# Optimization experiments

Measured on AMD Instinct MI355X. Metric: run time of the kernel, lower is better.

The kernel has to match this reference:

```python
import jax, jax.numpy as jnp
import numpy as np

B, T, DIM = 1, 1024, 1024
H = 8
QLR, KVLR = 768, 512
DNOPE, DROPE, DV = 128, 64, 128
DK = DNOPE + DROPE  # 192
EPS = 1e-5


def _rms(x, w):
    return x * jax.lax.rsqrt(jnp.mean(x * x, axis=-1, keepdims=True) + EPS) * w


def _l2norm(x):
    return x * jax.lax.rsqrt(jnp.sum(x * x, axis=-1, keepdims=True) + 1e-6)


def setup_inputs() -> dict:
    key = jax.random.key(0)
    ks = jax.random.split(key, 12)
    std = 0.02
    rnd = lambda k, shape: (jax.random.normal(k, shape, dtype=jnp.float32) * std)
    return {
        'x': jax.random.normal(ks[0], (B, T, DIM), dtype=jnp.float32),
        'cos': jax.random.normal(ks[1], (T, DROPE), dtype=jnp.float32),
        'sin': jax.random.normal(ks[2], (T, DROPE), dtype=jnp.float32),
        'wq_a': rnd(ks[3], (DIM, QLR)),
        'q_norm_w': jnp.ones((QLR,), dtype=jnp.float32),
        'wq_b': rnd(ks[4], (QLR, H * DK)),
        'wkv_a': rnd(ks[5], (DIM, KVLR + DROPE)),
        'kv_norm_w': jnp.ones((KVLR,), dtype=jnp.float32),
        'wkv_b': rnd(ks[6], (KVLR, H * (DNOPE + DV))),
        'wg_w': rnd(ks[7], (DIM, H * DK)),
        'wg_b': jnp.zeros((H * DK,), dtype=jnp.float32),
        'wb': rnd(ks[8], (DIM, H)),
        'wo': rnd(ks[9], (H * DV, DIM)),
    }


def _kda(q, k, v, g, beta):
    # q,k: [B,T,H,DK]; v: [B,T,H,DV]; g: [B,T,H,DK] (log-decay); beta: [B,T,H]
    q = _l2norm(q) * (DK ** -0.5)
    k = _l2norm(k)
    # time-major for scan
    qs = jnp.moveaxis(q, 1, 0)
    ks_ = jnp.moveaxis(k, 1, 0)
    vs = jnp.moveaxis(v, 1, 0)
    gs = jnp.moveaxis(g, 1, 0)
    bs = jnp.moveaxis(beta, 1, 0)

    def step(S, inp):
        q_t, k_t, v_t, g_t, b_t = inp  # [B,H,DK],[B,H,DK],[B,H,DV],[B,H,DK],[B,H]
        S = S * jnp.exp(g_t)[..., None]                       # per-key-dim decay
        u_t = b_t[..., None] * (v_t - jnp.einsum('bhk,bhkv->bhv', k_t, S))
        S = S + k_t[..., None] * u_t[..., None, :]            # rank-1 delta update
        o_t = jnp.einsum('bhk,bhkv->bhv', q_t, S)
        return S, o_t

    S0 = jnp.zeros((B, H, DK, DV), dtype=q.dtype)
    _, o = jax.lax.scan(step, S0, (qs, ks_, vs, gs, bs))
    return jnp.moveaxis(o, 0, 1)  # [B,T,H,DV]


def reference(x, cos, sin, wq_a, q_norm_w, wq_b, wkv_a, kv_norm_w, wkv_b, wg_w, wg_b, wb, wo):
    # cos/sin are accepted but unused, matching the original forward body.
    q = (_rms(x @ wq_a, q_norm_w) @ wq_b).reshape(B, T, H, DK)
    kv_all = x @ wkv_a
    kv_c, k_pe = kv_all[..., :KVLR], kv_all[..., KVLR:]       # [B,T,KVLR],[B,T,DROPE]
    kv = (_rms(kv_c, kv_norm_w) @ wkv_b).reshape(B, T, H, DNOPE + DV)
    k_nope, v = kv[..., :DNOPE], kv[..., DNOPE:]
    k = jnp.concatenate(
        [k_nope, jnp.broadcast_to(k_pe[:, :, None, :], (B, T, H, DROPE))], axis=-1)
    g = jax.nn.log_sigmoid(x @ wg_w + wg_b).reshape(B, T, H, DK)
    beta = jax.nn.sigmoid(x @ wb).reshape(B, T, H)
    o = _kda(q, k, v, g, beta)
    o = jnp.nan_to_num(o, nan=0.0, posinf=10000.0, neginf=-10000.0)
    return o.reshape(B, T, H * DV) @ wo
```

## Files before the change

### kernel.cpp

```cpp
#include <hip/hip_runtime.h>
#include <hip/hip_bf16.h>
#include <math.h>

#define TT 1024
#define DIM 1024
#define HH 8
#define QLR 768
#define KVLR 512
#define DNOPE 128
#define DROPE 64
#define DV 128
#define DK 192
#define HDK (HH*DK)
#define HKV (HH*(DNOPE+DV))

#define OY   0
#define OQ   3072
#define OC   6144
#define OPL  9984
#define OU   10240
#define OLAM 12288
#define PABLK 12480

typedef __attribute__((ext_vector_type(8))) short short8;
typedef __attribute__((ext_vector_type(4))) float f32x4;

__device__ __forceinline__ unsigned short f2bf_rn(float f) {
    unsigned u = __float_as_uint(f);
    unsigned lsb = (u >> 16) & 1u;
    u += 0x7fffu + lsb;
    return (unsigned short)(u >> 16);
}
__device__ __forceinline__ float bf2f(unsigned short h) {
    return __uint_as_float(((unsigned)h) << 16);
}

__global__ __launch_bounds__(256) void wconv(
    const float* __restrict__ W0, unsigned short* __restrict__ H0,
    unsigned short* __restrict__ L0, int K0, int N0, int T0,
    const float* __restrict__ W1, unsigned short* __restrict__ H1,
    unsigned short* __restrict__ L1, int K1, int N1, int T1,
    const float* __restrict__ W2, unsigned short* __restrict__ H2,
    unsigned short* __restrict__ L2, int K2, int N2, int T2)
{
    __shared__ float Ls[64][65];
    int bx = blockIdx.x;
    const float* W; unsigned short* H; unsigned short* L; int K, N;
    if (bx < T0)           { W = W0; H = H0; L = L0; K = K0; N = N0; }
    else if (bx < T0 + T1) { bx -= T0; W = W1; H = H1; L = L1; K = K1; N = N1; }
    else                   { bx -= T0 + T1; W = W2; H = H2; L = L2; K = K2; N = N2; }

    const int NT = N >> 6;
    const int kt = bx / NT, nt = bx - kt * NT;
    const int k0 = kt * 64, n0 = nt * 64;
    const int tid = threadIdx.x;
    const int r = tid >> 2, c = (tid & 3) * 16;

#pragma unroll
    for (int i = 0; i < 4; i++)
        *(float4*)&Ls[r][c + i * 4] =
            *(const float4*)&W[(size_t)(k0 + r) * N + n0 + c + i * 4];
    __syncthreads();

    const int nr = tid >> 2, kc = (tid & 3) * 16;
    unsigned short hb[16], lb[16];
#pragma unroll
    for (int j = 0; j < 16; j++) {
        float v = Ls[kc + j][nr];
        unsigned short h = f2bf_rn(v);
        hb[j] = h;
        lb[j] = f2bf_rn(v - bf2f(h));
    }
    size_t ob = (size_t)(n0 + nr) * K + k0 + kc;
    *(float4*)&H[ob]     = ((float4*)hb)[0];
    *(float4*)&H[ob + 8] = ((float4*)hb)[1];
    *(float4*)&L[ob]     = ((float4*)lb)[0];
    *(float4*)&L[ob + 8] = ((float4*)lb)[1];
}

__global__ __launch_bounds__(256) void aconv(
    const float* __restrict__ A, unsigned short* __restrict__ H,
    unsigned short* __restrict__ L)
{
    int i = (blockIdx.x * 256 + threadIdx.x) * 8;
    float4 v0 = *(const float4*)&A[i];
    float4 v1 = *(const float4*)&A[i + 4];
    float vv[8] = {v0.x, v0.y, v0.z, v0.w, v1.x, v1.y, v1.z, v1.w};
    unsigned short hb[8], lb[8];
#pragma unroll
    for (int j = 0; j < 8; j++) {
        unsigned short h = f2bf_rn(vv[j]);
        hb[j] = h;
        lb[j] = f2bf_rn(vv[j] - bf2f(h));
    }
    *(float4*)&H[i] = *(float4*)hb;
    *(float4*)&L[i] = *(float4*)lb;
}

__global__ __launch_bounds__(128) void gemm_bt(
    const unsigned short* __restrict__ Ah0, const unsigned short* __restrict__ Al0,
    const unsigned short* __restrict__ Bh0, const unsigned short* __restrict__ Bl0,
    float* __restrict__ C0, int K0, int N0, int T0,
    const unsigned short* __restrict__ Ah1, const unsigned short* __restrict__ Al1,
    const unsigned short* __restrict__ Bh1, const unsigned short* __restrict__ Bl1,
    float* __restrict__ C1, int K1, int N1, int T1,
    const unsigned short* __restrict__ Ah2, const unsigned short* __restrict__ Al2,
    const unsigned short* __restrict__ Bh2, const unsigned short* __restrict__ Bl2,
    float* __restrict__ C2, int K2, int N2, int T2)
{
    __shared__ unsigned short Ahs[64 * 40], Als[64 * 40];
    __shared__ unsigned short Bhs[64 * 40], Bls[64 * 40];

    int bx = blockIdx.x;
    const unsigned short *Ah, *Al, *Bh, *Bl; float* C; int K, N;
    if (bx < T0) {
        Ah = Ah0; Al = Al0; Bh = Bh0; Bl = Bl0; C = C0; K = K0; N = N0;
    } else if (bx < T0 + T1) {
        bx -= T0; Ah = Ah1; Al = Al1; Bh = Bh1; Bl = Bl1; C = C1; K = K1; N = N1;
    } else {
        bx -= T0 + T1; Ah = Ah2; Al = Al2; Bh = Bh2; Bl = Bl2; C = C2; K = K2; N = N2;
    }

    const int tid = threadIdx.x;
    const int w = tid >> 6, l = tid & 63;
    const int q = l >> 4, m16 = l & 15;
    const int bm = blockIdx.y * 64, bn = bx * 64;

    const int c0i = tid * 2, c1i = tid * 2 + 1;
    const int r0 = c0i >> 2, o0 = (c0i & 3) * 8;
    const int r1 = c1i >> 2, o1 = (c1i & 3) * 8;
    const unsigned short* pAh0 = Ah + (size_t)(bm + r0) * K + o0;
    const unsigned short* pAh1 = Ah + (size_t)(bm + r1) * K + o1;
    const unsigned short* pAl0 = Al + (size_t)(bm + r0) * K + o0;
    const unsigned short* pAl1 = Al + (size_t)(bm + r1) * K + o1;
    const unsigned short* pBh0 = Bh + (size_t)(bn + r0) * K + o0;
    const unsigned short* pBh1 = Bh + (size_t)(bn + r1) * K + o1;
    const unsigned short* pBl0 = Bl + (size_t)(bn + r0) * K + o0;
    const unsigned short* pBl1 = Bl + (size_t)(bn + r1) * K + o1;

    f32x4 acc[2][4];
#pragma unroll
    for (int i = 0; i < 2; i++)
#pragma unroll
        for (int j = 0; j < 4; j++)
            acc[i][j] = (f32x4){0.f, 0.f, 0.f, 0.f};

    float4 vAh0 = *(const float4*)pAh0, vAh1 = *(const float4*)pAh1;
    float4 vAl0 = *(const float4*)pAl0, vAl1 = *(const float4*)pAl1;
    float4 vBh0 = *(const float4*)pBh0, vBh1 = *(const float4*)pBh1;
    float4 vBl0 = *(const float4*)pBl0, vBl1 = *(const float4*)pBl1;

    for (int k0 = 0;; k0 += 32) {
        __syncthreads();
        *(float4*)&Ahs[r0 * 40 + o0] = vAh0; *(float4*)&Ahs[r1 * 40 + o1] = vAh1;
        *(float4*)&Als[r0 * 40 + o0] = vAl0; *(float4*)&Als[r1 * 40 + o1] = vAl1;
        *(float4*)&Bhs[r0 * 40 + o0] = vBh0; *(float4*)&Bhs[r1 * 40 + o1] = vBh1;
        *(float4*)&Bls[r0 * 40 + o0] = vBl0; *(float4*)&Bls[r1 * 40 + o1] = vBl1;
        __syncthreads();

        const bool more = (k0 + 32) < K;
        if (more) {
            const int kn = k0 + 32;
            vAh0 = *(const float4*)(pAh0 + kn); vAh1 = *(const float4*)(pAh1 + kn);
            vAl0 = *(const float4*)(pAl0 + kn); vAl1 = *(const float4*)(pAl1 + kn);
            vBh0 = *(const float4*)(pBh0 + kn); vBh1 = *(const float4*)(pBh1 + kn);
            vBl0 = *(const float4*)(pBl0 + kn); vBl1 = *(const float4*)(pBl1 + kn);
        }

        short8 fah[2], fal[2], fbh[4], fbl[4];
#pragma unroll
        for (int mt = 0; mt < 2; mt++) {
            const int row = w * 32 + mt * 16 + m16;
            fah[mt] = *(const short8*)&Ahs[row * 40 + q * 8];
            fal[mt] = *(const short8*)&Als[row * 40 + q * 8];
        }
#pragma unroll
        for (int nt = 0; nt < 4; nt++) {
            const int row = nt * 16 + m16;
            fbh[nt] = *(const short8*)&Bhs[row * 40 + q * 8];
            fbl[nt] = *(const short8*)&Bls[row * 40 + q * 8];
        }
#pragma unroll
        for (int mt = 0; mt < 2; mt++)
#pragma unroll
            for (int nt = 0; nt < 4; nt++) {
                acc[mt][nt] = __builtin_amdgcn_mfma_f32_16x16x32_bf16(
                    fah[mt], fbh[nt], acc[mt][nt], 0, 0, 0);
                acc[mt][nt] = __builtin_amdgcn_mfma_f32_16x16x32_bf16(
                    fah[mt], fbl[nt], acc[mt][nt], 0, 0, 0);
                acc[mt][nt] = __builtin_amdgcn_mfma_f32_16x16x32_bf16(
                    fal[mt], fbh[nt], acc[mt][nt], 0, 0, 0);
            }
        if (!more) break;
    }

#pragma unroll
    for (int mt = 0; mt < 2; mt++)
#pragma unroll
        for (int nt = 0; nt < 4; nt++) {
            const int mrow = bm + w * 32 + mt * 16 + q * 4;
            const int ncol = bn + nt * 16 + m16;
#pragma unroll
            for (int r = 0; r < 4; r++)
                C[(size_t)(mrow + r) * N + ncol] = acc[mt][nt][r];
        }
}

__global__ __launch_bounds__(256) void rmsnorm_bf2(
    const float* __restrict__ in0, const float* __restrict__ w0,
    unsigned short* __restrict__ oh0, unsigned short* __restrict__ ol0,
    const float* __restrict__ in1, const float* __restrict__ w1,
    unsigned short* __restrict__ oh1, unsigned short* __restrict__ ol1)
{
    int bx = blockIdx.x;
    const float* in; const float* w; unsigned short *oh, *ol;
    int t, stride, ncols; float inv_n;
    if (bx < TT) {
        t = bx; in = in0; w = w0; oh = oh0; ol = ol0;
        stride = QLR; ncols = QLR; inv_n = 1.f / QLR;
    } else {
        t = bx - TT; in = in1; w = w1; oh = oh1; ol = ol1;
        stride = KVLR + DROPE; ncols = KVLR; inv_n = 1.f / KVLR;
    }
    const int tid = threadIdx.x;
    const float* row = in + (size_t)t * stride;
    float ss = 0.f;
    for (int c = tid; c < ncols; c += 256) { float v = row[c]; ss += v * v; }
#pragma unroll
    for (int m = 1; m < 64; m <<= 1) ss += __shfl_xor(ss, m);
    __shared__ float red[4];
    if ((tid & 63) == 0) red[tid >> 6] = ss;
    __syncthreads();
    float tot = red[0] + red[1] + red[2] + red[3];
    float scale = rsqrtf(tot * inv_n + 1e-5f);
    for (int c = tid; c < ncols; c += 256) {
        float v = row[c] * scale * w[c];
        unsigned short h = f2bf_rn(v);
        oh[(size_t)t * ncols + c] = h;
        ol[(size_t)t * ncols + c] = f2bf_rn(v - bf2f(h));
    }
}

__global__ __launch_bounds__(256) void small_fused(
    const float* __restrict__ g, const float* __restrict__ bias,
    float* __restrict__ la_h,
    const float* __restrict__ x, const float* __restrict__ wb,
    float* __restrict__ betab,
    const float* __restrict__ qraw, const float* __restrict__ kvb,
    const float* __restrict__ kv_all, float* __restrict__ q_h,
    float* __restrict__ k_h)
{
    int bx = blockIdx.x;
    if (bx < 6144) {
        int i = bx * 256 + threadIdx.x;
        int t = i / HDK, col = i - t * HDK;
        int h = col / DK, d = col - h * DK;
        float z = g[i] + bias[col];
        float la = fminf(z, 0.f) - log1pf(__expf(-fabsf(z)));
        la_h[((size_t)h * TT + t) * DK + d] = la;
        return;
    }
    bx -= 6144;
    const int lane = threadIdx.x & 63, wv = threadIdx.x >> 6;
    if (bx < 2048) {
        const int p = bx * 4 + wv;
        const int t = p >> 3, h = p & 7;
        const float* xr = x + (size_t)t * DIM;
        float s = 0.f;
        for (int e = lane; e < DIM; e += 64) s += xr[e] * wb[e * HH + h];
#pragma unroll
        for (int m = 1; m < 64; m <<= 1) s += __shfl_xor(s, m);
        if (lane == 0) betab[p] = 1.f / (1.f + expf(-s));
        return;
    }
    bx -= 2048;
    {
        const int p = bx * 4 + wv;
        const int t = p >> 3, h = p & 7;

        const float* qrow = qraw + (size_t)t * HDK + h * DK;
        float q0 = qrow[lane], q1 = qrow[lane + 64], q2 = qrow[lane + 128];
        float ss = q0 * q0 + q1 * q1 + q2 * q2;
#pragma unroll
        for (int m = 1; m < 64; m <<= 1) ss += __shfl_xor(ss, m);
        float sc = rsqrtf(ss + 1e-6f) * 0.07216878364870323f;
        float* qo = q_h + ((size_t)h * TT + t) * DK;
        qo[lane] = q0 * sc; qo[lane + 64] = q1 * sc; qo[lane + 128] = q2 * sc;

        const float* knope = kvb + (size_t)t * HKV + h * (DNOPE + DV);
        float k0 = knope[lane], k1 = knope[lane + 64];
        float k2 = kv_all[(size_t)t * (KVLR + DROPE) + KVLR + lane];
        float ks = k0 * k0 + k1 * k1 + k2 * k2;
#pragma unroll
        for (int m = 1; m < 64; m <<= 1) ks += __shfl_xor(ks, m);
        float kc = rsqrtf(ks + 1e-6f);
        float* ko = k_h + ((size_t)h * TT + t) * DK;
        ko[lane] = k0 * kc; ko[lane + 64] = k1 * kc; ko[lane + 128] = k2 * kc;
    }
}

__device__ __forceinline__ float dpp_xor1(float x) {
    return __int_as_float(__builtin_amdgcn_update_dpp(
        0, __float_as_int(x), 0xB1, 0xF, 0xF, false));
}
__device__ __forceinline__ float dpp_xor2(float x) {
    return __int_as_float(__builtin_amdgcn_update_dpp(
        0, __float_as_int(x), 0x4E, 0xF, 0xF, false));
}
__device__ __forceinline__ float dpp_hm(float x) {
    return __int_as_float(__builtin_amdgcn_update_dpp(
        0, __float_as_int(x), 0x141, 0xF, 0xF, false));
}
__device__ __forceinline__ float red16(float x) {
    x += dpp_xor1(x);
    x += dpp_xor2(x);
    x += dpp_hm(x);
    x += __int_as_float(__builtin_amdgcn_update_dpp(0, __float_as_int(x), 0x140, 0xF, 0xF, false));
    return x;
}
__device__ __forceinline__ float red8(float x) {
    x += dpp_xor1(x);
    x += dpp_xor2(x);
    x += dpp_hm(x);
    return x;
}

__device__ __forceinline__ void gl_lds16(const float* g, float* l) {
    __builtin_amdgcn_global_load_lds(
        (const __attribute__((address_space(1))) void*)g,
        (__attribute__((address_space(3))) void*)l, 16, 0, 0);
}
__device__ __forceinline__ void gl_lds4(const float* g, float* l) {
    __builtin_amdgcn_global_load_lds(
        (const __attribute__((address_space(1))) void*)g,
        (__attribute__((address_space(3))) void*)l, 4, 0, 0);
}

__global__ __launch_bounds__(256) void chunk_prep(
    const float* __restrict__ k_h, const float* __restrict__ la_h,
    const float* __restrict__ q_h, const float* __restrict__ kvb,
    const float* __restrict__ betab, float* __restrict__ pa)
{
    __shared__ float Ls[16][196];
    __shared__ float Ks[16][196];
    __shared__ float Qs[16][196];
    __shared__ float Ws[16][196];
    __shared__ float Xs[16][196];
    __shared__ float Ms[16][16];
    __shared__ float bs[16];

    const int tid = threadIdx.x;
    const int n = blockIdx.x >> 3, h = blockIdx.x & 7;
    const size_t g0 = ((size_t)h * TT + n * 16) * DK;
    float* blob = pa + (size_t)blockIdx.x * PABLK;

#pragma unroll
    for (int s = 0; s < 3; s++) {
        int off = (tid * 3 + s) * 4;
        int r = off / 192, c = off - r * 192;
        *(float4*)&Ks[r][c] = *(const float4*)(k_h + g0 + off);
        *(float4*)&Ls[r][c] = *(const float4*)(la_h + g0 + off);
        *(float4*)&Qs[r][c] = *(const float4*)(q_h + g0 + off);
    }
    if (tid < 16) bs[tid] = betab[(size_t)(n * 16 + tid) * HH + h];
    __syncthreads();

    if (tid < 192) {
        float g = 0.f;
#pragma unroll
        for (int i = 0; i < 16; i++) { g += Ls[i][tid]; Ls[i][tid] = g; }
    }
    __syncthreads();

#pragma unroll
    for (int s = 0; s < 12; s++) {
        int idx = s * 256 + tid;
        int i = idx / 192, d = idx - i * 192;
        float G = Ls[i][d];
        float eg = __expf(G), en = __expf(-G);
        float kk = Ks[i][d];
        Ws[i][d] = bs[i] * kk * eg;
        Qs[i][d] *= eg;
        Ks[i][d] = kk * en;
    }
    __syncthreads();

#pragma unroll
    for (int s = 0; s < 3; s++) {
        int off = (tid * 3 + s) * 4;
        int r = off / 192, c = off - r * 192;
        *(float4*)(blob + OQ + off) = *(const float4*)&Qs[r][c];
    }
    if (tid < 192) {
        float lam = __expf(Ls[15][tid]);
        blob[OLAM + tid] = lam;
#pragma unroll
        for (int j4 = 0; j4 < 4; j4++) {
            float4 v;
            v.x = Ks[j4 * 4 + 0][tid] * lam; v.y = Ks[j4 * 4 + 1][tid] * lam;
            v.z = Ks[j4 * 4 + 2][tid] * lam; v.w = Ks[j4 * 4 + 3][tid] * lam;
            *(float4*)(blob + OC + tid * 20 + j4 * 4) = v;
        }
        blob[OC + tid * 20 + 16] = lam;
        blob[OC + tid * 20 + 17] = 0.f;
        blob[OC + tid * 20 + 18] = 0.f; blob[OC + tid * 20 + 19] = 0.f;
    }
    {
        const int i = tid >> 4, j = tid & 15;
        float m = 0.f, p = 0.f;
#pragma unroll
        for (int d4 = 0; d4 < 48; d4++) {
            float4 w  = *(const float4*)&Ws[i][d4 * 4];
            float4 ka = *(const float4*)&Ks[j][d4 * 4];
            float4 qa = *(const float4*)&Qs[i][d4 * 4];
            m += w.x * ka.x + w.y * ka.y + w.z * ka.z + w.w * ka.w;
            p += qa.x * ka.x + qa.y * ka.y + qa.z * ka.z + qa.w * ka.w;
        }
        Ms[i][j] = (j < i) ? m : 0.f;
        blob[OPL + tid] = (j <= i) ? p : 0.f;
    }
    __syncthreads();

    float y[16], uu[16];
    const bool doY = (tid < 192);
    const bool doU = (tid >= 128);
    const int dcol = tid, ccol = tid - 128;
    if (doY) {
#pragma unroll
        for (int i = 0; i < 16; i++) y[i] = Ws[i][dcol];
#pragma unroll
        for (int i = 1; i < 16; i++)
#pragma unroll
            for (int j = 0; j < i; j++)
                y[i] = fmaf(-Ms[i][j], y[j], y[i]);
    }
    if (doU) {
#pragma unroll
        for (int i = 0; i < 16; i++)
            uu[i] = bs[i] * kvb[(size_t)(n * 16 + i) * HKV + h * (DNOPE + DV) + DNOPE + ccol];
#pragma unroll
        for (int i = 1; i < 16; i++)
#pragma unroll
            for (int j = 0; j < i; j++)
                uu[i] = fmaf(-Ms[i][j], uu[j], uu[i]);
    }
    if (doY) {
#pragma unroll
        for (int i = 0; i < 16; i++) Xs[i][dcol] = y[i];
    }
    __syncthreads();
#pragma unroll
    for (int s = 0; s < 3; s++) {
        int off = (tid * 3 + s) * 4;
        int r = off / 192, c = off - r * 192;
        *(float4*)(blob + OY + off) = *(const float4*)&Xs[r][c];
    }
    __syncthreads();
    if (doU) {
#pragma unroll
        for (int i = 0; i < 16; i++) Xs[i][ccol] = uu[i];
    }
    __syncthreads();
#pragma unroll
    for (int s = 0; s < 2; s++) {
        int off = (tid * 2 + s) * 4;
        int r = off / 128, c = off - r * 128;
        *(float4*)(blob + OU + off) = *(const float4*)&Xs[r][c];
    }
}

__global__ __launch_bounds__(256) void kda_chunk(
    const float* __restrict__ pa, unsigned short* __restrict__ obh,
    unsigned short* __restrict__ obl)
{
    __shared__ float Cb[3][3840];
    __shared__ float Pb[3][256];
    __shared__ float ubs[3][32];
    __shared__ float lbs[3][192];
    __shared__ float Ss[392];
    __shared__ float us[40];

    const int tid = threadIdx.x;
    const int w = tid >> 6, lane = tid & 63;
    const int h = blockIdx.x & 7, cg = blockIdx.x >> 3;
    const int c0 = cg * 2;

    const int dg  = tid & 15;
    const int cc  = (tid >> 4) & 1;
    const int tig = tid >> 5;
    const int dbase = dg * 12;

    auto stage = [&](int buf, int n) {
        const float* blob = pa + (size_t)(n * 8 + h) * PABLK;
        if (w == 0) {
#pragma unroll
            for (int s = 0; s < 8; s++)
                gl_lds16(blob + OC + s * 256 + lane * 4, &Cb[buf][s * 256]);
        } else if (w == 1) {
#pragma unroll
            for (int s = 8; s < 15; s++)
                gl_lds16(blob + OC + s * 256 + lane * 4, &Cb[buf][s * 256]);
        } else if (w == 2) {
            gl_lds16(blob + OPL + lane * 4, &Pb[buf][0]);
            if (lane < 32)
                gl_lds4(blob + OU + (lane >> 1) * 128 + c0 + (lane & 1), &ubs[buf][0]);
            if (lane < 48)
                gl_lds16(blob + OLAM + lane * 4, &lbs[buf][0]);
        }
    };

    auto ldYQ = [&](int n, float4 (&Y)[2][3], float4 (&Q)[2][3]) {
        const float* blob = pa + (size_t)(n * 8 + h) * PABLK;
#pragma unroll
        for (int i = 0; i < 2; i++) {
            const float* py = blob + OY + (tig * 2 + i) * 192 + dbase;
            const float* pq = blob + OQ + (tig * 2 + i) * 192 + dbase;
#pragma unroll
            for (int s = 0; s < 3; s++) {
                Y[i][s] = *(const float4*)(py + s * 4);
                Q[i][s] = *(const float4*)(pq + s * 4);
            }
        }
    };

    for (int idx = tid; idx < 392; idx += 256) Ss[idx] = 0.f;
    stage(0, 0);
    stage(1, 1);

    float4 YA[2][3], QA[2][3], YB[2][3], QB[2][3];
    ldYQ(0, YA, QA);

    const int c2 = tid & 1, dseg = tid >> 1;

    auto body = [&](int n, int bf, float4 (&Yc)[2][3], float4 (&Qc)[2][3],
                    float4 (&Yn)[2][3], float4 (&Qn)[2][3]) {
        __syncthreads();

        if (n + 2 < TT / 16) {
            int b2 = bf + 2; if (b2 >= 3) b2 -= 3;
            stage(b2, n + 2);
        }
        {
            int np = n + 1; if (np > TT / 16 - 1) np = TT / 16 - 1;
            ldYQ(np, Yn, Qn);
        }

        float4 sv[3];
#pragma unroll
        for (int s = 0; s < 3; s++)
            sv[s] = *(const float4*)&Ss[cc * 196 + dbase + s * 4];

        float py[2] = {0.f, 0.f};
        float pq[2] = {0.f, 0.f};
#pragma unroll
        for (int i = 0; i < 2; i++)
#pragma unroll
            for (int s = 0; s < 3; s++) {
                float4 yv = Yc[i][s];
                float4 qv = Qc[i][s];
                float4 s4 = sv[s];
                py[i] = fmaf(yv.x, s4.x, py[i]);
                py[i] = fmaf(yv.y, s4.y, py[i]);
                py[i] = fmaf(yv.z, s4.z, py[i]);
                py[i] = fmaf(yv.w, s4.w, py[i]);
                pq[i] = fmaf(qv.x, s4.x, pq[i]);
                pq[i] = fmaf(qv.y, s4.y, pq[i]);
                pq[i] = fmaf(qv.z, s4.z, pq[i]);
                pq[i] = fmaf(qv.w, s4.w, pq[i]);
            }
        float zy[2], zq[2];
#pragma unroll
        for (int i = 0; i < 2; i++) {
            zy[i] = red16(py[i]);
            zq[i] = red16(pq[i]);
        }

        float uv[2];
#pragma unroll
        for (int i = 0; i < 2; i++)
            uv[i] = ubs[bf][(tig * 2 + i) * 2 + cc] - zy[i];
        if ((dg & 7) == 0) {
            const int ii = dg >> 3;
            us[cc * 20 + tig * 2 + ii] = (ii == 0) ? uv[0] : uv[1];
        }
        __syncthreads();

        {
            const int ii = dg >> 3, qtr = dg & 7;
            const int ti = tig * 2 + ii;
            float acc = 0.f;
#pragma unroll
            for (int j = qtr; j <= 15; j += 8)
                if (j <= ti) acc = fmaf(Pb[bf][ti * 16 + j], us[cc * 20 + j], acc);
            acc = red8(acc);
            if (qtr == 0) {
                float ov = zq[ii] + acc;
                if (isnan(ov)) ov = 0.f;
                else if (isinf(ov)) ov = ov > 0.f ? 1e4f : -1e4f;
                size_t oi = (size_t)(n * 16 + ti) * (HH * DV) + h * DV + c0 + cc;
                unsigned short hb = f2bf_rn(ov);
                obh[oi] = hb;
                obl[oi] = f2bf_rn(ov - bf2f(hb));
            }
        }

        if (tid < 128) {
            const float4* up = (const float4*)&us[c2 * 20];
            float4 u0 = up[0], u1 = up[1], u2v = up[2], u3 = up[3];
#pragma unroll
            for (int s = 0; s < 3; s++) {
                int d = dseg * 3 + s;
                float svv = Ss[c2 * 196 + d];
                float a2 = lbs[bf][d] * svv;
                const float4* C4 = (const float4*)&Cb[bf][d * 20];
                float4 k0 = C4[0], k1 = C4[1], k2 = C4[2], k3 = C4[3];
                a2 = fmaf(k0.x, u0.x,  a2); a2 = fmaf(k0.y, u0.y,  a2);
                a2 = fmaf(k0.z, u0.z,  a2); a2 = fmaf(k0.w, u0.w,  a2);
                a2 = fmaf(k1.x, u1.x,  a2); a2 = fmaf(k1.y, u1.y,  a2);
                a2 = fmaf(k1.z, u1.z,  a2); a2 = fmaf(k1.w, u1.w,  a2);
                a2 = fmaf(k2.x, u2v.x, a2); a2 = fmaf(k2.y, u2v.y, a2);
                a2 = fmaf(k2.z, u2v.z, a2); a2 = fmaf(k2.w, u2v.w, a2);
                a2 = fmaf(k3.x, u3.x,  a2); a2 = fmaf(k3.y, u3.y,  a2);
                a2 = fmaf(k3.z, u3.z,  a2); a2 = fmaf(k3.w, u3.w,  a2);
                Ss[c2 * 196 + d] = a2;
            }
        }
    };

    int buf = 0;
    for (int n = 0; n < TT / 16; n += 2) {
        body(n, buf, YA, QA, YB, QB);
        int b1 = buf + 1; if (b1 >= 3) b1 -= 3;
        body(n + 1, b1, YB, QB, YA, QA);
        buf += 2; if (buf >= 3) buf -= 3;
    }
}

extern "C" void kernel_launch(void* const* d_in, const int* in_sizes, int n_in,
                              void* d_out, int out_size, void* d_ws, size_t ws_size,
                              hipStream_t stream)
{
    const float* x         = (const float*)d_in[0];
    const float* wq_a      = (const float*)d_in[3];
    const float* q_norm_w  = (const float*)d_in[4];
    const float* wq_b      = (const float*)d_in[5];
    const float* wkv_a     = (const float*)d_in[6];
    const float* kv_norm_w = (const float*)d_in[7];
    const float* wkv_b     = (const float*)d_in[8];
    const float* wg_w      = (const float*)d_in[9];
    const float* wg_b      = (const float*)d_in[10];
    const float* wb        = (const float*)d_in[11];
    const float* wo        = (const float*)d_in[12];
    float* out = (float*)d_out;

    float* ws = (float*)d_ws;
    float* xq     = ws;
    float* kv_all = xq     + TT * QLR;
    float* agraw  = kv_all + TT * (KVLR + DROPE);
    float* qnraw  = agraw  + TT * HDK;
    float* kvb    = qnraw  + TT * HDK;
    float* la_h   = kvb    + TT * HKV;
    float* q_h    = la_h   + TT * HDK;
    float* k_h    = q_h    + TT * HDK;
    float* betab  = k_h    + TT * HDK;
    float* pa     = betab  + TT * HH;
    float* tail   = pa     + 512 * PABLK;

    unsigned short* wo_h  = (unsigned short*)tail;
    unsigned short* wo_l  = wo_h  + 1048576;
    unsigned short* xh    = wo_l  + 1048576;
    unsigned short* xl    = xh    + 1048576;
    unsigned short* xqh   = xl    + 1048576;
    unsigned short* xql   = xqh   + 786432;
    unsigned short* kvnh  = xql   + 786432;
    unsigned short* kvnl  = kvnh  + 524288;

    unsigned short* wqa_h  = (unsigned short*)pa;
    unsigned short* wqa_l  = wqa_h  + 786432;
    unsigned short* wkva_h = wqa_l  + 786432;
    unsigned short* wkva_l = wkva_h + 589824;
    unsigned short* wgw_h  = wkva_l + 589824;
    unsigned short* wgw_l  = wgw_h  + 1572864;
    unsigned short* wqb_h  = wgw_l  + 1572864;
    unsigned short* wqb_l  = wqb_h  + 1179648;
    unsigned short* wkvb_h = wqb_l  + 1179648;
    unsigned short* wkvb_l = wkvb_h + 1048576;

    unsigned short* obh = (unsigned short*)agraw;
    unsigned short* obl = obh + 1048576;

    dim3 blk(256);

    wconv<<<dim3(192 + 144 + 384), blk, 0, stream>>>(
        wq_a, wqa_h, wqa_l, DIM, QLR, 192,
        wkv_a, wkva_h, wkva_l, DIM, KVLR + DROPE, 144,
        wg_w, wgw_h, wgw_l, DIM, HDK, 384);
    wconv<<<dim3(288 + 256 + 256), blk, 0, stream>>>(
        wq_b, wqb_h, wqb_l, QLR, HDK, 288,
        wkv_b, wkvb_h, wkvb_l, KVLR, HKV, 256,
        wo, wo_h, wo_l, DIM, DIM, 256);

    aconv<<<dim3(TT * DIM / (256 * 8)), blk, 0, stream>>>(x, xh, xl);

    gemm_bt<<<dim3(12 + 9 + 24, 16), dim3(128), 0, stream>>>(
        xh, xl, wqa_h, wqa_l, xq, DIM, QLR, 12,
        xh, xl, wkva_h, wkva_l, kv_all, DIM, KVLR + DROPE, 9,
        xh, xl, wgw_h, wgw_l, agraw, DIM, HDK, 24);

    rmsnorm_bf2<<<dim3(2 * TT), blk, 0, stream>>>(
        xq, q_norm_w, xqh, xql,
        kv_all, kv_norm_w, kvnh, kvnl);

    gemm_bt<<<dim3(24 + 32, 16), dim3(128), 0, stream>>>(
        xqh, xql, wqb_h, wqb_l, qnraw, QLR, HDK, 24,
        kvnh, kvnl, wkvb_h, wkvb_l, kvb, KVLR, HKV, 32,
        xh, xl, wqa_h, wqa_l, xq, DIM, QLR, 0);

    small_fused<<<dim3(6144 + 2048 + 2048), blk, 0, stream>>>(
        agraw, wg_b, la_h,
        x, wb, betab,
        qnraw, kvb, kv_all, q_h, k_h);

    chunk_prep<<<512, blk, 0, stream>>>(k_h, la_h, q_h, kvb, betab, pa);
    kda_chunk<<<512, blk, 0, stream>>>(pa, obh, obl);

    gemm_bt<<<dim3(16, 16), dim3(128), 0, stream>>>(
        obh, obl, wo_h, wo_l, out, DIM, DIM, 16,
        xh, xl, wqa_h, wqa_l, xq, DIM, QLR, 0,
        xh, xl, wqa_h, wqa_l, xq, DIM, QLR, 0);
}
```

Baseline: 315.0 us.

## Double kda_chunk block to 512 threads, one row per thread group

Raises the recurrent chunk kernel's block from 256 to 512 threads. Each 32-thread group now handles one time row instead of two, the triangular P·u product uses all 16 lanes with a 16-wide reduction, and the state update spreads 384 threads over one key dimension each instead of 128 threads looping over three. Staging loads are redistributed across six waves. This shortens the serial per-chunk critical path, at the cost of more threads synchronising at each barrier and possibly lower occupancy per CU.

New measurement: 316.4 us. About the same (+0.5%).

```diff
diff --git a/kernel.cpp b/kernel.cpp
--- a/kernel.cpp
+++ b/kernel.cpp
@@ -318,12 +318,6 @@
     x += __int_as_float(__builtin_amdgcn_update_dpp(0, __float_as_int(x), 0x140, 0xF, 0xF, false));
     return x;
 }
-__device__ __forceinline__ float red8(float x) {
-    x += dpp_xor1(x);
-    x += dpp_xor2(x);
-    x += dpp_hm(x);
-    return x;
-}
 
 __device__ __forceinline__ void gl_lds16(const float* g, float* l) {
     __builtin_amdgcn_global_load_lds(
@@ -469,7 +463,7 @@
     }
 }
 
-__global__ __launch_bounds__(256) void kda_chunk(
+__global__ __launch_bounds__(512, 4) void kda_chunk(
     const float* __restrict__ pa, unsigned short* __restrict__ obh,
     unsigned short* __restrict__ obl)
 {
@@ -492,16 +486,18 @@
 
     auto stage = [&](int buf, int n) {
         const float* blob = pa + (size_t)(n * 8 + h) * PABLK;
-        if (w == 0) {
-#pragma unroll
-            for (int s = 0; s < 8; s++)
+        if (w < 3) {
+#pragma unroll
+            for (int s = 0; s < 4; s++)
+                gl_lds16(blob + OC + (w * 4 + s) * 256 + lane * 4,
+                         &Cb[buf][(w * 4 + s) * 256]);
+        } else if (w == 3) {
+#pragma unroll
+            for (int s = 12; s < 15; s++)
                 gl_lds16(blob + OC + s * 256 + lane * 4, &Cb[buf][s * 256]);
-        } else if (w == 1) {
-#pragma unroll
-            for (int s = 8; s < 15; s++)
-                gl_lds16(blob + OC + s * 256 + lane * 4, &Cb[buf][s * 256]);
-        } else if (w == 2) {
+        } else if (w == 4) {
             gl_lds16(blob + OPL + lane * 4, &Pb[buf][0]);
+        } else if (w == 5) {
             if (lane < 32)
                 gl_lds4(blob + OU + (lane >> 1) * 128 + c0 + (lane & 1), &ubs[buf][0]);
             if (lane < 48)
@@ -509,31 +505,26 @@
         }
     };
 
-    auto ldYQ = [&](int n, float4 (&Y)[2][3], float4 (&Q)[2][3]) {
+    auto ldYQ = [&](int n, float4 (&Y)[3], float4 (&Q)[3]) {
         const float* blob = pa + (size_t)(n * 8 + h) * PABLK;
-#pragma unroll
-        for (int i = 0; i < 2; i++) {
-            const float* py = blob + OY + (tig * 2 + i) * 192 + dbase;
-            const float* pq = blob + OQ + (tig * 2 + i) * 192 + dbase;
-#pragma unroll
-            for (int s = 0; s < 3; s++) {
-                Y[i][s] = *(const float4*)(py + s * 4);
-                Q[i][s] = *(const float4*)(pq + s * 4);
-            }
+        const float* py_ = blob + OY + tig * 192 + dbase;
+        const float* pq_ = blob + OQ + tig * 192 + dbase;
+#pragma unroll
+        for (int s = 0; s < 3; s++) {
+            Y[s] = *(const float4*)(py_ + s * 4);
+            Q[s] = *(const float4*)(pq_ + s * 4);
         }
     };
 
-    for (int idx = tid; idx < 392; idx += 256) Ss[idx] = 0.f;
+    for (int idx = tid; idx < 392; idx += 512) Ss[idx] = 0.f;
     stage(0, 0);
     stage(1, 1);
 
-    float4 YA[2][3], QA[2][3], YB[2][3], QB[2][3];
+    float4 YA[3], QA[3], YB[3], QB[3];
     ldYQ(0, YA, QA);
 
-    const int c2 = tid & 1, dseg = tid >> 1;
-
-    auto body = [&](int n, int bf, float4 (&Yc)[2][3], float4 (&Qc)[2][3],
-                    float4 (&Yn)[2][3], float4 (&Qn)[2][3]) {
+    auto body = [&](int n, int bf, float4 (&Yc)[3], float4 (&Qc)[3],
+                    float4 (&Yn)[3], float4 (&Qn)[3]) {
         __syncthreads();
 
         if (n + 2 < TT / 16) {
@@ -550,80 +541,60 @@
         for (int s = 0; s < 3; s++)
             sv[s] = *(const float4*)&Ss[cc * 196 + dbase + s * 4];
 
-        float py[2] = {0.f, 0.f};
-        float pq[2] = {0.f, 0.f};
-#pragma unroll
-        for (int i = 0; i < 2; i++)
-#pragma unroll
-            for (int s = 0; s < 3; s++) {
-                float4 yv = Yc[i][s];
-                float4 qv = Qc[i][s];
-                float4 s4 = sv[s];
-                py[i] = fmaf(yv.x, s4.x, py[i]);
-                py[i] = fmaf(yv.y, s4.y, py[i]);
-                py[i] = fmaf(yv.z, s4.z, py[i]);
-                py[i] = fmaf(yv.w, s4.w, py[i]);
-                pq[i] = fmaf(qv.x, s4.x, pq[i]);
-                pq[i] = fmaf(qv.y, s4.y, pq[i]);
-                pq[i] = fmaf(qv.z, s4.z, pq[i]);
-                pq[i] = fmaf(qv.w, s4.w, pq[i]);
-            }
-        float zy[2], zq[2];
-#pragma unroll
-        for (int i = 0; i < 2; i++) {
-            zy[i] = red16(py[i]);
-            zq[i] = red16(pq[i]);
-        }
-
-        float uv[2];
-#pragma unroll
-        for (int i = 0; i < 2; i++)
-            uv[i] = ubs[bf][(tig * 2 + i) * 2 + cc] - zy[i];
-        if ((dg & 7) == 0) {
-            const int ii = dg >> 3;
-            us[cc * 20 + tig * 2 + ii] = (ii == 0) ? uv[0] : uv[1];
-        }
+        float py = 0.f, pq = 0.f;
+#pragma unroll
+        for (int s = 0; s < 3; s++) {
+            float4 yv = Yc[s];
+            float4 qv = Qc[s];
+            float4 s4 = sv[s];
+            py = fmaf(yv.x, s4.x, py);
+            py = fmaf(yv.y, s4.y, py);
+            py = fmaf(yv.z, s4.z, py);
+            py = fmaf(yv.w, s4.w, py);
+            pq = fmaf(qv.x, s4.x, pq);
+            pq = fmaf(qv.y, s4.y, pq);
+            pq = fmaf(qv.z, s4.z, pq);
+            pq = fmaf(qv.w, s4.w, pq);
+        }
+        float zy = red16(py);
+        float zq = red16(pq);
+
+        float uv = ubs[bf][tig * 2 + cc] - zy;
+        if (dg == 0) us[cc * 20 + tig] = uv;
         __syncthreads();
 
         {
-            const int ii = dg >> 3, qtr = dg & 7;
-            const int ti = tig * 2 + ii;
-            float acc = 0.f;
-#pragma unroll
-            for (int j = qtr; j <= 15; j += 8)
-                if (j <= ti) acc = fmaf(Pb[bf][ti * 16 + j], us[cc * 20 + j], acc);
-            acc = red8(acc);
-            if (qtr == 0) {
-                float ov = zq[ii] + acc;
+            float acc = (dg <= tig) ? Pb[bf][tig * 16 + dg] * us[cc * 20 + dg]
+                                    : 0.f;
+            acc = red16(acc);
+            if (dg == 0) {
+                float ov = zq + acc;
                 if (isnan(ov)) ov = 0.f;
                 else if (isinf(ov)) ov = ov > 0.f ? 1e4f : -1e4f;
-                size_t oi = (size_t)(n * 16 + ti) * (HH * DV) + h * DV + c0 + cc;
+                size_t oi = (size_t)(n * 16 + tig) * (HH * DV) + h * DV + c0 + cc;
                 unsigned short hb = f2bf_rn(ov);
                 obh[oi] = hb;
                 obl[oi] = f2bf_rn(ov - bf2f(hb));
             }
         }
 
-        if (tid < 128) {
+        if (tid < 384) {
+            const int d = tid >> 1, c2 = tid & 1;
             const float4* up = (const float4*)&us[c2 * 20];
             float4 u0 = up[0], u1 = up[1], u2v = up[2], u3 = up[3];
-#pragma unroll
-            for (int s = 0; s < 3; s++) {
-                int d = dseg * 3 + s;
-                float svv = Ss[c2 * 196 + d];
-                float a2 = lbs[bf][d] * svv;
-                const float4* C4 = (const float4*)&Cb[bf][d * 20];
-                float4 k0 = C4[0], k1 = C4[1], k2 = C4[2], k3 = C4[3];
-                a2 = fmaf(k0.x, u0.x,  a2); a2 = fmaf(k0.y, u0.y,  a2);
-                a2 = fmaf(k0.z, u0.z,  a2); a2 = fmaf(k0.w, u0.w,  a2);
-                a2 = fmaf(k1.x, u1.x,  a2); a2 = fmaf(k1.y, u1.y,  a2);
-                a2 = fmaf(k1.z, u1.z,  a2); a2 = fmaf(k1.w, u1.w,  a2);
-                a2 = fmaf(k2.x, u2v.x, a2); a2 = fmaf(k2.y, u2v.y, a2);
-                a2 = fmaf(k2.z, u2v.z, a2); a2 = fmaf(k2.w, u2v.w, a2);
-                a2 = fmaf(k3.x, u3.x,  a2); a2 = fmaf(k3.y, u3.y,  a2);
-                a2 = fmaf(k3.z, u3.z,  a2); a2 = fmaf(k3.w, u3.w,  a2);
-                Ss[c2 * 196 + d] = a2;
-            }
+            float svv = Ss[c2 * 196 + d];
+            float a2 = lbs[bf][d] * svv;
+            const float4* C4 = (const float4*)&Cb[bf][d * 20];
+            float4 k0 = C4[0], k1 = C4[1], k2 = C4[2], k3 = C4[3];
+            a2 = fmaf(k0.x, u0.x,  a2); a2 = fmaf(k0.y, u0.y,  a2);
+            a2 = fmaf(k0.z, u0.z,  a2); a2 = fmaf(k0.w, u0.w,  a2);
+            a2 = fmaf(k1.x, u1.x,  a2); a2 = fmaf(k1.y, u1.y,  a2);
+            a2 = fmaf(k1.z, u1.z,  a2); a2 = fmaf(k1.w, u1.w,  a2);
+            a2 = fmaf(k2.x, u2v.x, a2); a2 = fmaf(k2.y, u2v.y, a2);
+            a2 = fmaf(k2.z, u2v.z, a2); a2 = fmaf(k2.w, u2v.w, a2);
+            a2 = fmaf(k3.x, u3.x,  a2); a2 = fmaf(k3.y, u3.y,  a2);
+            a2 = fmaf(k3.z, u3.z,  a2); a2 = fmaf(k3.w, u3.w,  a2);
+            Ss[c2 * 196 + d] = a2;
         }
     };
 
@@ -722,7 +693,7 @@
         qnraw, kvb, kv_all, q_h, k_h);
 
     chunk_prep<<<512, blk, 0, stream>>>(k_h, la_h, q_h, kvb, betab, pa);
-    kda_chunk<<<512, blk, 0, stream>>>(pa, obh, obl);
+    kda_chunk<<<512, dim3(512), 0, stream>>>(pa, obh, obl);
 
     gemm_bt<<<dim3(16, 16), dim3(128), 0, stream>>>(
         obh, obl, wo_h, wo_l, out, DIM, DIM, 16,
```
